# Kernel optimization log

Hardware: AMD Instinct MI355X
Metric: run time of the kernel (lower is better)

The kernel has to match this reference:

```python
import jax, jax.numpy as jnp
import numpy as np

EPS = 1e-5
K = 1  # kernel_size; forced to 1 by the module's channel bookkeeping (see notes)


def conv2d(x, w, stride=1, padding=0):
    return jax.lax.conv_general_dilated(
        x, w, (stride, stride), [(padding, padding), (padding, padding)],
        dimension_numbers=('NCHW', 'OIHW', 'NCHW'))


def bn_eval(x, g, b):
    # eval-mode BatchNorm2d with running_mean=0, running_var=1
    scale = g * np.float32(1.0 / np.sqrt(1.0 + EPS))
    return x * scale.reshape(1, -1, 1, 1) + b.reshape(1, -1, 1, 1)


def spdconv(x, w, g, b):
    # SPDConv: 2x2 space-to-depth -> conv (bias=False) -> BN -> SiLU
    s2d = jnp.concatenate([x[..., ::2, ::2], x[..., 1::2, ::2],
                           x[..., ::2, 1::2], x[..., 1::2, 1::2]], axis=1)
    return jax.nn.silu(bn_eval(conv2d(s2d, w), g, b))


def fourier_split(x):
    # Fourierforward(J=1): zero-pad to next pow2, rfft2, split low/high bands
    h, w = x.shape[-2], x.shape[-1]
    ph = 1 << int(np.ceil(np.log2(h)))
    pw = 1 << int(np.ceil(np.log2(w)))
    xp = jnp.pad(x, ((0, 0), (0, 0), (0, ph - h), (0, pw - w)))
    f = jnp.fft.rfft2(xp)
    low = f[:, :, :h // 2 + 1, :w // 2 + 1]
    high = f[:, :, h // 2 + 1:h + 1, :w // 2 + 1]
    return low.real, low.imag, high.real, high.imag


def sdi(x, w, b):
    # SDI1: per-sample (unbatched) 3x3 conv, then cumulative product over the batch dim
    y = conv2d(x, w, padding=1) + b.reshape(1, -1, 1, 1)
    return jnp.cumprod(y, axis=0)


def fourier_sdi(x, sdi_w, sdi_b, fuse_w, fuse_g, fuse_b):
    yl, y1, y2, y3 = fourier_split(x)
    parts = [sdi(t, sdi_w, sdi_b) for t in (yl, y1, y2, y3)]
    cat = jnp.concatenate(parts, axis=1)  # (b, 4, h', w')
    return jax.nn.silu(bn_eval(conv2d(cat, fuse_w), fuse_g, fuse_b))


def _forward(x, w_spd_gw, bn_g_gw, bn_b_gw, sdi_w_gw, sdi_b_gw, fuse_w_gw, fuse_g_gw, fuse_b_gw,
             w_spd_gf, bn_g_gf, bn_b_gf, sdi_w_gf, sdi_b_gf, fuse_w_gf, fuse_g_gf, fuse_b_gf,
             gen_g, gen_b, w_final):
    b, c = x.shape[0], x.shape[1]
    # get_weight branch: SPDConv(1x1) -> Fourier_SDIModel
    weight = fourier_sdi(spdconv(x, w_spd_gw, bn_g_gw, bn_b_gw),
                         sdi_w_gw, sdi_b_gw, fuse_w_gw, fuse_g_gw, fuse_b_gw)
    h, w = weight.shape[2], weight.shape[3]
    weighted = jax.nn.softmax(weight.reshape(b, c * c, K * K, h, w), axis=2)
    # generate_feature branch: SPDConv(k) -> Fourier_SDIModel -> BN -> ReLU
    feat = fourier_sdi(spdconv(x, w_spd_gf, bn_g_gf, bn_b_gf),
                       sdi_w_gf, sdi_b_gf, fuse_w_gf, fuse_g_gf, fuse_b_gf)
    feat = jax.nn.relu(bn_eval(feat, gen_g, gen_b)).reshape(b, c * c, K * K, h, w)
    wd = feat * weighted
    # rearrange 'b c (n1 n2) h w -> b c (h n1) (w n2)'
    conv_data = wd.reshape(b, c * c, K, K, h, w).transpose(0, 1, 4, 2, 5, 3)
    conv_data = conv_data.reshape(b, c * c, h * K, w * K)
    # final conv: kernel K, stride autopad(K, p=K)=K (passed as stride arg), no bias
    return conv2d(conv_data, w_final, stride=K)


def setup_inputs() -> dict:
    key = jax.random.key(0)
    ks = jax.random.split(key, 24)
    n = lambda i, shape, s=1.0: jax.random.normal(ks[i], shape, dtype=jnp.float32) * s
    # sdi 3x3 weights scaled ~1/(fft_magnitude*taps) so the cumulative product over
    # the batch dim stays in fp32 range.
    return {
        'x': n(0, (16, 1, 1022, 1022)),
        'w_spd_gw': n(1, (1, 4, 1, 1), 0.5),
        'bn_g_gw': 1.0 + n(2, (1,), 0.1),
        'bn_b_gw': n(3, (1,), 0.1),
        'sdi_w_gw': n(4, (1, 1, 3, 3), 5e-4),
        'sdi_b_gw': n(5, (1,), 0.01),
        'fuse_w_gw': n(6, (1, 4, 1, 1), 0.3),
        'fuse_g_gw': 1.0 + n(7, (1,), 0.1),
        'fuse_b_gw': n(8, (1,), 0.1),
        'w_spd_gf': n(9, (1, 4, 1, 1), 0.5),
        'bn_g_gf': 1.0 + n(10, (1,), 0.1),
        'bn_b_gf': n(11, (1,), 0.1),
        'sdi_w_gf': n(12, (1, 1, 3, 3), 5e-4),
        'sdi_b_gf': n(13, (1,), 0.01),
        'fuse_w_gf': n(14, (1, 4, 1, 1), 0.3),
        'fuse_g_gf': 1.0 + n(15, (1,), 0.1),
        'fuse_b_gf': n(16, (1,), 0.1),
        'gen_g': 1.0 + n(17, (1,), 0.1),
        'gen_b': n(18, (1,), 0.1),
        'w_final': n(19, (64, 1, 1, 1), 0.1),
    }


def reference(x, w_spd_gw, bn_g_gw, bn_b_gw, sdi_w_gw, sdi_b_gw, fuse_w_gw, fuse_g_gw, fuse_b_gw,
              w_spd_gf, bn_g_gf, bn_b_gf, sdi_w_gf, sdi_b_gf, fuse_w_gf, fuse_g_gf, fuse_b_gf,
              gen_g, gen_b, w_final):
    return _forward(x, w_spd_gw, bn_g_gw, bn_b_gw, sdi_w_gw, sdi_b_gw, fuse_w_gw, fuse_g_gw, fuse_b_gw,
                    w_spd_gf, bn_g_gf, bn_b_gf, sdi_w_gf, sdi_b_gf, fuse_w_gf, fuse_g_gf, fuse_b_gf,
                    gen_g, gen_b, w_final)
```

## Files before the change

kernel.cpp:

```cpp
#include <hip/hip_runtime.h>
#include <math.h>


#define PI_F 3.14159265358979323846f

struct cpx { float re, im; };
__device__ __forceinline__ cpx cadd(cpx a, cpx b){ return {a.re+b.re, a.im+b.im}; }
__device__ __forceinline__ cpx csub(cpx a, cpx b){ return {a.re-b.re, a.im-b.im}; }
__device__ __forceinline__ cpx cmul(cpx a, cpx b){ return {a.re*b.re - a.im*b.im, a.re*b.im + a.im*b.re}; }
__device__ __forceinline__ cpx cnegi(cpx a){ return {a.im, -a.re}; }

__device__ __forceinline__ void dft8_dif(cpx* a) {
    const float C = 0.70710678118654752440f;
    cpx t0=cadd(a[0],a[4]), t1=cadd(a[1],a[5]), t2=cadd(a[2],a[6]), t3=cadd(a[3],a[7]);
    cpx s0=csub(a[0],a[4]), s1=csub(a[1],a[5]), s2=csub(a[2],a[6]), s3=csub(a[3],a[7]);
    s1 = (cpx){ C*(s1.re + s1.im), C*(s1.im - s1.re) };
    s2 = cnegi(s2);
    s3 = (cpx){ C*(s3.im - s3.re), -C*(s3.re + s3.im) };
    cpx u0=cadd(t0,t2), u1=cadd(t1,t3), u2=csub(t0,t2), u3=cnegi(csub(t1,t3));
    cpx v0=cadd(s0,s2), v1=cadd(s1,s3), v2=csub(s0,s2), v3=cnegi(csub(s1,s3));
    a[0]=cadd(u0,u1); a[1]=csub(u0,u1); a[2]=cadd(u2,u3); a[3]=csub(u2,u3);
    a[4]=cadd(v0,v1); a[5]=csub(v0,v1); a[6]=cadd(v2,v3); a[7]=csub(v2,v3);
}

__device__ __forceinline__ void twiddle_brev(cpx* a, cpx p) {
    cpx w = p;
    a[4] = cmul(a[4], w); w = cmul(w, p);
    a[2] = cmul(a[2], w); w = cmul(w, p);
    a[6] = cmul(a[6], w); w = cmul(w, p);
    a[1] = cmul(a[1], w); w = cmul(w, p);
    a[5] = cmul(a[5], w); w = cmul(w, p);
    a[3] = cmul(a[3], w); w = cmul(w, p);
    a[7] = cmul(a[7], w);
}

__device__ __forceinline__ void fft512_r8(cpx* a, float* bR, float* bI, int t) {
    float sn, cs;
    dft8_dif(a);
    sincosf(-2.0f * PI_F * (float)t / 512.0f, &sn, &cs);
    twiddle_brev(a, (cpx){cs, sn});
    bR[0*69 + t] = a[0].re; bI[0*69 + t] = a[0].im;
    bR[4*69 + t] = a[1].re; bI[4*69 + t] = a[1].im;
    bR[2*69 + t] = a[2].re; bI[2*69 + t] = a[2].im;
    bR[6*69 + t] = a[3].re; bI[6*69 + t] = a[3].im;
    bR[1*69 + t] = a[4].re; bI[1*69 + t] = a[4].im;
    bR[5*69 + t] = a[5].re; bI[5*69 + t] = a[5].im;
    bR[3*69 + t] = a[6].re; bI[3*69 + t] = a[6].im;
    bR[7*69 + t] = a[7].re; bI[7*69 + t] = a[7].im;
    __syncthreads();
    int k0 = t & 7, t0 = t >> 3;
    cpx b[8];
#pragma unroll
    for (int i = 0; i < 8; i++) {
        b[i].re = bR[k0*69 + t0 + 8*i];
        b[i].im = bI[k0*69 + t0 + 8*i];
    }
    __syncthreads();
    dft8_dif(b);
    sincosf(-2.0f * PI_F * (float)t0 / 64.0f, &sn, &cs);
    twiddle_brev(b, (cpx){cs, sn});
    bR[(0*8 + k0)*9 + t0] = b[0].re; bI[(0*8 + k0)*9 + t0] = b[0].im;
    bR[(4*8 + k0)*9 + t0] = b[1].re; bI[(4*8 + k0)*9 + t0] = b[1].im;
    bR[(2*8 + k0)*9 + t0] = b[2].re; bI[(2*8 + k0)*9 + t0] = b[2].im;
    bR[(6*8 + k0)*9 + t0] = b[3].re; bI[(6*8 + k0)*9 + t0] = b[3].im;
    bR[(1*8 + k0)*9 + t0] = b[4].re; bI[(1*8 + k0)*9 + t0] = b[4].im;
    bR[(5*8 + k0)*9 + t0] = b[5].re; bI[(5*8 + k0)*9 + t0] = b[5].im;
    bR[(3*8 + k0)*9 + t0] = b[6].re; bI[(3*8 + k0)*9 + t0] = b[6].im;
    bR[(7*8 + k0)*9 + t0] = b[7].re; bI[(7*8 + k0)*9 + t0] = b[7].im;
    __syncthreads();
    int rowb = ((t >> 3) * 8 + (t & 7)) * 9;
#pragma unroll
    for (int i = 0; i < 8; i++) {
        a[i].re = bR[rowb + i];
        a[i].im = bI[rowb + i];
    }
    __syncthreads();
    dft8_dif(a);
}

__global__ __launch_bounds__(512) void fft_rows_spd8(
        const float* __restrict__ x, const float* __restrict__ w4,
        const float* __restrict__ g1, const float* __restrict__ b1,
        float2* __restrict__ RT) {
    __shared__ __align__(16) float pool[9216];
    int tid = threadIdx.x;
    int w = tid >> 6, t = tid & 63;
    float* bR = pool + w * 1152;
    float* bI = bR + 576;
    int row = blockIdx.x * 8 + w;
    int b = row >> 9, yy = row & 511;
    float w0 = w4[0], w1 = w4[1], w2c = w4[2], w3 = w4[3];
    float scale = g1[0] * rsqrtf(1.f + 1e-5f);
    float bias  = b1[0];
    cpx a[8];
#pragma unroll
    for (int m = 0; m < 8; m++) {
        int p = t + 64 * m;
        float v = 0.f;
        if (yy < 511 && p < 511) {
            const float* r0 = x + ((size_t)b * 1022 + 2 * yy) * 1022 + 2 * p;
            float2 e = *(const float2*)r0;
            float2 o = *(const float2*)(r0 + 1022);
            v = w0 * e.x + w1 * o.x + w2c * e.y + w3 * o.y;
            v = v * scale + bias;
            v = v / (1.f + expf(-v));
        }
        a[m] = (cpx){v, 0.f};
    }
    fft512_r8(a, bR, bI, t);
    float2* tile = (float2*)pool;
    tile[(t +   0) * 9 + w] = make_float2(a[0].re, a[0].im);
    tile[(t +  64) * 9 + w] = make_float2(a[4].re, a[4].im);
    tile[(t + 128) * 9 + w] = make_float2(a[2].re, a[2].im);
    tile[(t + 192) * 9 + w] = make_float2(a[6].re, a[6].im);
    __syncthreads();
    int y0 = (blockIdx.x & 63) * 8;
    float2* dst = RT + (size_t)(b * 256) * 512 + y0;
#pragma unroll
    for (int r = 0; r < 4; r++) {
        int e = tid + 512 * r;
        int k = e >> 3, ww = e & 7;
        dst[(size_t)k * 512 + ww] = tile[k * 9 + ww];
    }
}

__global__ __launch_bounds__(512) void fft_cols8(
        const float2* __restrict__ RT, float* __restrict__ tpl) {
    __shared__ __align__(16) float pool[9216];
    int tid = threadIdx.x;
    int w = tid >> 6, t = tid & 63;
    float* bR = pool + w * 1152;
    float* bI = bR + 576;
    int b = blockIdx.x >> 5;
    int kx0 = (blockIdx.x & 31) * 8;
    const float2* src = RT + (size_t)(b * 256 + kx0 + w) * 512;
    cpx a[8];
#pragma unroll
    for (int m = 0; m < 8; m++) {
        float2 v = src[t + 64 * m];
        a[m] = (cpx){v.x, v.y};
    }
    fft512_r8(a, bR, bI, t);
    float2* tile = (float2*)pool;
    tile[(t +   0) * 9 + w] = make_float2(a[0].re, a[0].im);
    tile[(t +  64) * 9 + w] = make_float2(a[4].re, a[4].im);
    tile[(t + 128) * 9 + w] = make_float2(a[2].re, a[2].im);
    tile[(t + 192) * 9 + w] = make_float2(a[6].re, a[6].im);
    tile[(t + 256) * 9 + w] = make_float2(a[1].re, a[1].im);
    tile[(t + 320) * 9 + w] = make_float2(a[5].re, a[5].im);
    tile[(t + 384) * 9 + w] = make_float2(a[3].re, a[3].im);
    tile[(t + 448) * 9 + w] = make_float2(a[7].re, a[7].im);
    __syncthreads();
    const size_t P = (size_t)16 * 256 * 256;
#pragma unroll
    for (int r = 0; r < 8; r++) {
        int e = tid + 512 * r;
        int ky = e >> 3, ww = e & 7;
        float2 v = tile[ky * 9 + ww];
        if (ky < 256) {
            size_t idx = (size_t)(b * 256 + ky) * 256 + kx0 + ww;
            tpl[idx]     = v.x;
            tpl[P + idx] = v.y;
        } else {
            size_t idx = (size_t)(b * 256 + (ky - 256)) * 256 + kx0 + ww;
            tpl[2*P + idx] = v.x;
            tpl[3*P + idx] = v.y;
        }
    }
}

__global__ void conv_y_k(const float* __restrict__ tpl,
                         const float* __restrict__ sdiw,
                         const float* __restrict__ sdib,
                         float* __restrict__ y) {
    int idx = blockIdx.x * 256 + threadIdx.x;
    int j = idx & 255, i = (idx >> 8) & 255;
    const float* base = tpl + ((size_t)(idx >> 16)) * 65536;
    float acc = sdib[0];
    float w9[9];
#pragma unroll
    for (int k = 0; k < 9; k++) w9[k] = sdiw[k];
#pragma unroll
    for (int di = 0; di < 3; di++) {
        int ii = i + di - 1;
        if (ii < 0 || ii > 255) continue;
        const float* rowp = base + (size_t)ii * 256;
#pragma unroll
        for (int dj = 0; dj < 3; dj++) {
            int jj = j + dj - 1;
            if (jj < 0 || jj > 255) continue;
            acc += w9[di * 3 + dj] * rowp[jj];
        }
    }
    y[idx] = acc;
}

__global__ __launch_bounds__(256) void cum_expand(
        const float* __restrict__ y,
        const float* __restrict__ fw, const float* __restrict__ fg,
        const float* __restrict__ fb, const float* __restrict__ gg,
        const float* __restrict__ gb, const float* __restrict__ wf,
        float* __restrict__ out) {
    int og = blockIdx.x & 1;
    int pix = (blockIdx.x >> 1) * 256 + threadIdx.x;
    float v[16][4];
#pragma unroll
    for (int b = 0; b < 16; b++)
#pragma unroll
        for (int c = 0; c < 4; c++)
            v[b][c] = y[((size_t)(c * 16 + b)) * 65536 + pix];
    float inv = rsqrtf(1.f + 1e-5f);
    float fscale = fg[0] * inv, fbias = fb[0];
    float gscale = gg[0] * inv, gbias = gb[0];
    float fw0 = fw[0], fw1 = fw[1], fw2 = fw[2], fw3 = fw[3];
    float f2[16];
    float p0 = 1.f, p1 = 1.f, p2 = 1.f, p3 = 1.f;
#pragma unroll
    for (int b = 0; b < 16; b++) {
        p0 *= v[b][0]; p1 *= v[b][1]; p2 *= v[b][2]; p3 *= v[b][3];
        float f = fw0 * p0 + fw1 * p1 + fw2 * p2 + fw3 * p3;
        float bn = f * fscale + fbias;
        float ft = bn / (1.f + expf(-bn));
        float g = ft * gscale + gbias;
        f2[b] = fmaxf(g, 0.f);
    }
    for (int oo = 0; oo < 32; oo++) {
        int o = og * 32 + oo;
        float s = wf[o];
#pragma unroll
        for (int b = 0; b < 16; b++)
            out[((size_t)(b * 64 + o)) * 65536 + pix] = f2[b] * s;
    }
}

extern "C" void kernel_launch(void* const* d_in, const int* in_sizes, int n_in,
                              void* d_out, int out_size, void* d_ws, size_t ws_size,
                              hipStream_t stream) {
    const float* x    = (const float*)d_in[0];
    const float* wspd = (const float*)d_in[9];
    const float* bng  = (const float*)d_in[10];
    const float* bnb  = (const float*)d_in[11];
    const float* sdiw = (const float*)d_in[12];
    const float* sdib = (const float*)d_in[13];
    const float* fw   = (const float*)d_in[14];
    const float* fg   = (const float*)d_in[15];
    const float* fb   = (const float*)d_in[16];
    const float* gg   = (const float*)d_in[17];
    const float* gb   = (const float*)d_in[18];
    const float* wf   = (const float*)d_in[19];
    float* out = (float*)d_out;

    float2* RT  = (float2*)d_ws;
    float*  tpl = (float*)d_ws + (size_t)4 * 1024 * 1024;
    float*  y   = (float*)d_ws;

    fft_rows_spd8<<<dim3(1024),  dim3(512), 0, stream>>>(x, wspd, bng, bnb, RT);
    fft_cols8    <<<dim3(512),   dim3(512), 0, stream>>>(RT, tpl);
    conv_y_k     <<<dim3(16384), dim3(256), 0, stream>>>(tpl, sdiw, sdib, y);
    cum_expand   <<<dim3(512),   dim3(256), 0, stream>>>(y, fw, fg, fb, gg, gb, wf, out);
}
```

Before: 400.0 us.

## Fuse SDI 3x3 conv into cumprod/expand kernel with shared-memory tiles

Merges the standalone 3x3 conv kernel into the cumulative-product/expand kernel. Each block stages a 16x16 tile plus halo for the four bands in shared memory per batch step and computes the conv on the fly, so the intermediate y buffer is never written to or read back from global memory. It also swaps sincosf for the faster __sincosf intrinsic in the FFT twiddles and simplifies a row index. The costs are per-batch shared-memory staging with two barriers per step, some halo overfetch, and lower twiddle precision.

```diff
diff --git a/kernel.cpp b/kernel.cpp
--- a/kernel.cpp
+++ b/kernel.cpp
@@ -37,7 +37,7 @@
 __device__ __forceinline__ void fft512_r8(cpx* a, float* bR, float* bI, int t) {
     float sn, cs;
     dft8_dif(a);
-    sincosf(-2.0f * PI_F * (float)t / 512.0f, &sn, &cs);
+    __sincosf(-2.0f * PI_F * (float)t / 512.0f, &sn, &cs);
     twiddle_brev(a, (cpx){cs, sn});
     bR[0*69 + t] = a[0].re; bI[0*69 + t] = a[0].im;
     bR[4*69 + t] = a[1].re; bI[4*69 + t] = a[1].im;
@@ -57,7 +57,7 @@
     }
     __syncthreads();
     dft8_dif(b);
-    sincosf(-2.0f * PI_F * (float)t0 / 64.0f, &sn, &cs);
+    __sincosf(-2.0f * PI_F * (float)t0 / 64.0f, &sn, &cs);
     twiddle_brev(b, (cpx){cs, sn});
     bR[(0*8 + k0)*9 + t0] = b[0].re; bI[(0*8 + k0)*9 + t0] = b[0].im;
     bR[(4*8 + k0)*9 + t0] = b[1].re; bI[(4*8 + k0)*9 + t0] = b[1].im;
@@ -68,7 +68,7 @@
     bR[(3*8 + k0)*9 + t0] = b[6].re; bI[(3*8 + k0)*9 + t0] = b[6].im;
     bR[(7*8 + k0)*9 + t0] = b[7].re; bI[(7*8 + k0)*9 + t0] = b[7].im;
     __syncthreads();
-    int rowb = ((t >> 3) * 8 + (t & 7)) * 9;
+    int rowb = t * 9;
 #pragma unroll
     for (int i = 0; i < 8; i++) {
         a[i].re = bR[rowb + i];
@@ -169,67 +169,75 @@
     }
 }
 
-__global__ void conv_y_k(const float* __restrict__ tpl,
-                         const float* __restrict__ sdiw,
-                         const float* __restrict__ sdib,
-                         float* __restrict__ y) {
-    int idx = blockIdx.x * 256 + threadIdx.x;
-    int j = idx & 255, i = (idx >> 8) & 255;
-    const float* base = tpl + ((size_t)(idx >> 16)) * 65536;
-    float acc = sdib[0];
-    float w9[9];
-#pragma unroll
-    for (int k = 0; k < 9; k++) w9[k] = sdiw[k];
-#pragma unroll
-    for (int di = 0; di < 3; di++) {
-        int ii = i + di - 1;
-        if (ii < 0 || ii > 255) continue;
-        const float* rowp = base + (size_t)ii * 256;
-#pragma unroll
-        for (int dj = 0; dj < 3; dj++) {
-            int jj = j + dj - 1;
-            if (jj < 0 || jj > 255) continue;
-            acc += w9[di * 3 + dj] * rowp[jj];
-        }
-    }
-    y[idx] = acc;
-}
-
-__global__ __launch_bounds__(256) void cum_expand(
-        const float* __restrict__ y,
+__global__ __launch_bounds__(256) void conv_cum_expand(
+        const float* __restrict__ tpl,
+        const float* __restrict__ sdiw, const float* __restrict__ sdib,
         const float* __restrict__ fw, const float* __restrict__ fg,
         const float* __restrict__ fb, const float* __restrict__ gg,
         const float* __restrict__ gb, const float* __restrict__ wf,
         float* __restrict__ out) {
-    int og = blockIdx.x & 1;
-    int pix = (blockIdx.x >> 1) * 256 + threadIdx.x;
-    float v[16][4];
-#pragma unroll
-    for (int b = 0; b < 16; b++)
-#pragma unroll
-        for (int c = 0; c < 4; c++)
-            v[b][c] = y[((size_t)(c * 16 + b)) * 65536 + pix];
+    __shared__ float tile[4][18][20];
+    int tt  = threadIdx.x;
+    int og  = blockIdx.x & 1;
+    int tix = blockIdx.x >> 1;
+    int ti0 = (tix >> 4) * 16, tj0 = (tix & 15) * 16;
+    int tin = tt >> 4, tjn = tt & 15;
+    int gi_c = ti0 + tin, gj_c = tj0 + tjn;
+
+    float w9[9];
+#pragma unroll
+    for (int k = 0; k < 9; k++) w9[k] = sdiw[k];
+    float bias = sdib[0];
     float inv = rsqrtf(1.f + 1e-5f);
     float fscale = fg[0] * inv, fbias = fb[0];
     float gscale = gg[0] * inv, gbias = gb[0];
-    float fw0 = fw[0], fw1 = fw[1], fw2 = fw[2], fw3 = fw[3];
-    float f2[16];
-    float p0 = 1.f, p1 = 1.f, p2 = 1.f, p3 = 1.f;
-#pragma unroll
+    float fw4[4] = {fw[0], fw[1], fw[2], fw[3]};
+    float wfv[32];
+#pragma unroll
+    for (int oo = 0; oo < 32; oo++) wfv[oo] = wf[og * 32 + oo];
+
+    const size_t P = (size_t)16 * 65536;
+    float p[4] = {1.f, 1.f, 1.f, 1.f};
+    float* obase = out + (size_t)gi_c * 256 + gj_c;
+
     for (int b = 0; b < 16; b++) {
-        p0 *= v[b][0]; p1 *= v[b][1]; p2 *= v[b][2]; p3 *= v[b][3];
-        float f = fw0 * p0 + fw1 * p1 + fw2 * p2 + fw3 * p3;
+#pragma unroll
+        for (int it = 0; it < 6; it++) {
+            int id = it * 256 + tt;
+            if (id < 1296) {
+                int c  = id / 324;
+                int rm = id - c * 324;
+                int r  = rm / 18;
+                int cc = rm - r * 18;
+                int gi = ti0 + r - 1, gj = tj0 + cc - 1;
+                float v = 0.f;
+                if (gi >= 0 && gi < 256 && gj >= 0 && gj < 256)
+                    v = tpl[c * P + (size_t)b * 65536 + gi * 256 + gj];
+                tile[c][r][cc] = v;
+            }
+        }
+        __syncthreads();
+        float f = 0.f;
+#pragma unroll
+        for (int c = 0; c < 4; c++) {
+            float acc = bias;
+#pragma unroll
+            for (int di = 0; di < 3; di++)
+#pragma unroll
+                for (int dj = 0; dj < 3; dj++)
+                    acc += w9[di * 3 + dj] * tile[c][tin + di][tjn + dj];
+            p[c] *= acc;
+            f += fw4[c] * p[c];
+        }
         float bn = f * fscale + fbias;
         float ft = bn / (1.f + expf(-bn));
-        float g = ft * gscale + gbias;
-        f2[b] = fmaxf(g, 0.f);
-    }
-    for (int oo = 0; oo < 32; oo++) {
-        int o = og * 32 + oo;
-        float s = wf[o];
-#pragma unroll
-        for (int b = 0; b < 16; b++)
-            out[((size_t)(b * 64 + o)) * 65536 + pix] = f2[b] * s;
+        float g  = ft * gscale + gbias;
+        float f2 = fmaxf(g, 0.f);
+        float* ob = obase + (size_t)(b * 64 + og * 32) * 65536;
+#pragma unroll
+        for (int oo = 0; oo < 32; oo++)
+            ob[(size_t)oo * 65536] = f2 * wfv[oo];
+        __syncthreads();
     }
 }
 
@@ -252,10 +260,9 @@
 
     float2* RT  = (float2*)d_ws;
     float*  tpl = (float*)d_ws + (size_t)4 * 1024 * 1024;
-    float*  y   = (float*)d_ws;
-
-    fft_rows_spd8<<<dim3(1024),  dim3(512), 0, stream>>>(x, wspd, bng, bnb, RT);
-    fft_cols8    <<<dim3(512),   dim3(512), 0, stream>>>(RT, tpl);
-    conv_y_k     <<<dim3(16384), dim3(256), 0, stream>>>(tpl, sdiw, sdib, y);
-    cum_expand   <<<dim3(512),   dim3(256), 0, stream>>>(y, fw, fg, fb, gg, gb, wf, out);
-}
+
+    fft_rows_spd8  <<<dim3(1024), dim3(512), 0, stream>>>(x, wspd, bng, bnb, RT);
+    fft_cols8      <<<dim3(512),  dim3(512), 0, stream>>>(RT, tpl);
+    conv_cum_expand<<<dim3(512),  dim3(256), 0, stream>>>(tpl, sdiw, sdib, fw, fg,
+                                                          fb, gg, gb, wf, out);
+}
```

New measurement: 402.1 us. Within noise of the previous version (+0.5%).
